# Optimization experiments

Measured on AMD Instinct MI355X. Metric: run time of the kernel, lower is better.

The kernel has to match this reference:

```python
import jax, jax.numpy as jnp
import numpy as np

B, S, D = 4, 2048, 1024
LN_EPS = 1e-3  # Keras LayerNormalization default epsilon

def setup_inputs() -> dict:
    key = jax.random.key(0)
    ks = jax.random.split(key, 7)
    s = D ** -0.5
    return {
        "x": jax.random.normal(ks[0], (B, S, D), dtype=jnp.float32),
        "Wq": jax.random.normal(ks[1], (D, D), dtype=jnp.float32) * s,
        "bq": jnp.zeros((D,), dtype=jnp.float32),
        "Wk": jax.random.normal(ks[2], (D, D), dtype=jnp.float32) * s,
        "bk": jnp.zeros((D,), dtype=jnp.float32),
        "Wv": jax.random.normal(ks[3], (D, D), dtype=jnp.float32) * s,
        "bv": jnp.zeros((D,), dtype=jnp.float32),
        "gamma": jnp.ones((D,), dtype=jnp.float32),
        "beta": jnp.zeros((D,), dtype=jnp.float32),
    }

def reference(x, Wq, bq, Wk, bk, Wv, bv, gamma, beta):
    q = jnp.einsum('bsd,de->bse', x, Wq) + bq
    k = jnp.einsum('bsd,de->bse', x, Wk) + bk
    v = jnp.einsum('bsd,de->bse', x, Wv) + bv
    scale = jnp.asarray(k.shape[-1], x.dtype) ** -0.5
    scores = jnp.einsum('bqd,bkd->bqk', q, k) * scale  # [B,S,S]
    weights = jax.nn.softmax(scores, axis=-1)
    attn = jnp.einsum('bqk,bkd->bqd', weights, v)
    h = x + attn
    mu = jnp.mean(h, axis=-1, keepdims=True)
    var = jnp.mean(jnp.square(h - mu), axis=-1, keepdims=True)
    return gamma * (h - mu) * jax.lax.rsqrt(var + LN_EPS) + beta
```

## Files before the change

### kernel.cpp

```cpp
#include <hip/hip_runtime.h>

typedef __attribute__((ext_vector_type(8))) short bf16x8;
typedef __attribute__((ext_vector_type(4))) float f32x4;

__device__ __forceinline__ unsigned short f2bf(float f) {
    union { float f; unsigned int u; } v; v.f = f;
    unsigned int u = v.u;
    u += 0x7fffu + ((u >> 16) & 1u);
    return (unsigned short)(u >> 16);
}
__device__ __forceinline__ float bf2f(unsigned short s) {
    union { unsigned int u; float f; } v; v.u = ((unsigned int)s) << 16;
    return v.f;
}

__device__ __forceinline__ void gload16(const unsigned short* g, unsigned short* l) {
    __builtin_amdgcn_global_load_lds(
        (const __attribute__((address_space(1))) unsigned int*)(unsigned long long)(g),
        (__attribute__((address_space(3))) unsigned int*)(unsigned int)(unsigned long long)(l),
        16, 0, 0);
}

#define MFMA16(a, b, c) __builtin_amdgcn_mfma_f32_16x16x32_bf16((a), (b), (c), 0, 0, 0)

__global__ __launch_bounds__(256) void detect_dtype(
    const unsigned short* __restrict__ x, int* __restrict__ flag) {
    __shared__ int red[4];
    const int t = threadIdx.x;
    int cnt = 0;
    #pragma unroll
    for (int i = 0; i < 16; i++) {
        const unsigned short v = x[t * 16 + i];
        const int e = (v >> 7) & 0xFF;
        cnt += (e >= 0xC8) ? 1 : 0;
    }
    #pragma unroll
    for (int off = 32; off; off >>= 1) cnt += __shfl_down(cnt, off);
    if ((t & 63) == 0) red[t >> 6] = cnt;
    __syncthreads();
    if (t == 0) *flag = (red[0] + red[1] + red[2] + red[3] >= 16) ? 1 : 0;
}

__global__ __launch_bounds__(256) void convert_x(
    const void* __restrict__ xin, unsigned short* __restrict__ xb,
    const int* __restrict__ flag) {
    const long i = ((long)blockIdx.x * 256 + threadIdx.x) * 4;
    if (*flag) {
        const float4 v = *(const float4*)((const float*)xin + i);
        unsigned long long pk =  (unsigned long long)f2bf(v.x)
                              | ((unsigned long long)f2bf(v.y) << 16)
                              | ((unsigned long long)f2bf(v.z) << 32)
                              | ((unsigned long long)f2bf(v.w) << 48);
        *(unsigned long long*)(xb + i) = pk;
    } else {
        *(unsigned long long*)(xb + i) =
            *(const unsigned long long*)((const unsigned short*)xin + i);
    }
}

__global__ __launch_bounds__(256) void transpose_convert(
    const void* __restrict__ W, unsigned short* __restrict__ Wt,
    const int* __restrict__ flag) {
    __shared__ unsigned short tile[32][33];
    const int tx = threadIdx.x & 31, ty = threadIdx.x >> 5;
    const int x0 = blockIdx.x * 32, y0 = blockIdx.y * 32;
    const int f = *flag;
    #pragma unroll
    for (int i = 0; i < 32; i += 8) {
        const long idx = (long)(y0 + ty + i) * 1024 + x0 + tx;
        tile[ty + i][tx] = f ? f2bf(((const float*)W)[idx])
                             : ((const unsigned short*)W)[idx];
    }
    __syncthreads();
    #pragma unroll
    for (int i = 0; i < 32; i += 8)
        Wt[(long)(x0 + ty + i) * 1024 + y0 + tx] = tile[tx][ty + i];
}

__global__ __launch_bounds__(256) void convert_vec1024(
    const void* __restrict__ in, unsigned short* __restrict__ outv,
    const int* __restrict__ flag) {
    const int i = threadIdx.x * 4;
    if (*flag) {
        const float4 v = *(const float4*)((const float*)in + i);
        outv[i] = f2bf(v.x); outv[i+1] = f2bf(v.y);
        outv[i+2] = f2bf(v.z); outv[i+3] = f2bf(v.w);
    } else {
        *(unsigned long long*)(outv + i) =
            *(const unsigned long long*)((const unsigned short*)in + i);
    }
}

__global__ __launch_bounds__(512, 2) void gemm_bt(
    const unsigned short* __restrict__ A, const unsigned short* __restrict__ Bt,
    unsigned short* __restrict__ C,
    int K, int lda, int ldb, int ldc,
    long strideAz, long strideBz, long strideCz,
    const unsigned short* __restrict__ bias, float scale) {

    const int gx = gridDim.x, gy = gridDim.y;
    const int nwg = gx * gy * (int)gridDim.z;
    int bid = (int)blockIdx.x + gx * ((int)blockIdx.y + gy * (int)blockIdx.z);
    {
        const int q = nwg >> 3, r = nwg & 7;
        const int xcd = bid & 7, idx = bid >> 3;
        bid = (xcd < r ? xcd * (q + 1) : r * (q + 1) + (xcd - r) * q) + idx;
    }
    const int bz  = bid / (gx * gy);
    const int rmd = bid - bz * gx * gy;
    const int by  = rmd / gx;
    const int bx  = rmd - by * gx;

    A  += (long)bz * strideAz;
    Bt += (long)bz * strideBz;
    C  += (long)bz * strideCz;

    __shared__ unsigned short lds[73728];

    const int tid  = threadIdx.x;
    const int wave = tid >> 6;
    const int lane = tid & 63;
    const int quad = lane >> 4;
    const int lm   = lane & 15;
    const int wm   = (wave >> 2) * 64;
    const int wn   = (wave & 3) * 64;

    const int m0 = by * 128;
    const int n0 = bx * 256;

    const int rl   = wave * 8 + (lane >> 3);
    const int ksrc = (((lane & 7) ^ ((lane >> 3) & 7)) << 3);
    const unsigned short* pA0 = A  + (long)(m0 + rl) * lda + ksrc;
    const unsigned short* pB0 = Bt + (long)(n0 + rl) * ldb + ksrc;
    const long sA1 = 64L * lda, sB1 = 64L * ldb;
    const int wofs = wave * 512;

    const int sx8 = lm & 7;
    const int kq0 = ((quad ^ sx8) << 3);
    const int kq1 = (((4 + quad) ^ sx8) << 3);
    const int aro = (wm + lm) << 6;
    const int bro = (wn + lm) << 6;

    f32x4 acc[4][4];
    #pragma unroll
    for (int i = 0; i < 4; i++)
        #pragma unroll
        for (int j = 0; j < 4; j++) acc[i][j] = (f32x4){0.f, 0.f, 0.f, 0.f};

    const int NT = K >> 6;

#define STAGE(kt) do {                                                    \
        unsigned short* ab_ = &lds[((kt) % 3) * 24576 + wofs];            \
        unsigned short* bb_ = ab_ + 8192;                                 \
        const unsigned short* ga_ = pA0 + (long)(kt) * 64;                \
        const unsigned short* gb_ = pB0 + (long)(kt) * 64;                \
        gload16(ga_,            ab_);                                     \
        gload16(ga_ + sA1,      ab_ + 4096);                              \
        gload16(gb_,            bb_);                                     \
        gload16(gb_ + sB1,      bb_ + 4096);                              \
        gload16(gb_ + 2 * sB1,  bb_ + 8192);                              \
        gload16(gb_ + 3 * sB1,  bb_ + 12288);                             \
    } while (0)

    STAGE(0); STAGE(1);
    asm volatile("s_waitcnt vmcnt(6)" ::: "memory");
    __builtin_amdgcn_s_barrier();

    for (int kt = 0; kt < NT; ++kt) {
        const unsigned short* ab = &lds[(kt % 3) * 24576];
        const unsigned short* bb = ab + 8192;

        if (kt + 2 < NT) STAGE(kt + 2);

        bf16x8 aM[4][2], bN[2][2], bN2[2][2];
        #pragma unroll
        for (int i = 0; i < 4; i++) {
            aM[i][0] = *(const bf16x8*)&ab[aro + (i << 10) + kq0];
            aM[i][1] = *(const bf16x8*)&ab[aro + (i << 10) + kq1];
        }
        #pragma unroll
        for (int j = 0; j < 2; j++) {
            bN[j][0] = *(const bf16x8*)&bb[bro + (j << 10) + kq0];
            bN[j][1] = *(const bf16x8*)&bb[bro + (j << 10) + kq1];
        }
        __builtin_amdgcn_s_setprio(1);
        #pragma unroll
        for (int i = 0; i < 4; i++)
            #pragma unroll
            for (int j = 0; j < 2; j++) {
                acc[i][j] = MFMA16(aM[i][0], bN[j][0], acc[i][j]);
                acc[i][j] = MFMA16(aM[i][1], bN[j][1], acc[i][j]);
            }
        __builtin_amdgcn_s_setprio(0);
        #pragma unroll
        for (int j = 0; j < 2; j++) {
            bN2[j][0] = *(const bf16x8*)&bb[bro + ((j + 2) << 10) + kq0];
            bN2[j][1] = *(const bf16x8*)&bb[bro + ((j + 2) << 10) + kq1];
        }
        __builtin_amdgcn_s_setprio(1);
        #pragma unroll
        for (int i = 0; i < 4; i++)
            #pragma unroll
            for (int j = 0; j < 2; j++) {
                acc[i][j + 2] = MFMA16(aM[i][0], bN2[j][0], acc[i][j + 2]);
                acc[i][j + 2] = MFMA16(aM[i][1], bN2[j][1], acc[i][j + 2]);
            }
        __builtin_amdgcn_s_setprio(0);

        if (kt + 2 < NT) { asm volatile("s_waitcnt vmcnt(6)" ::: "memory"); }
        else             { asm volatile("s_waitcnt vmcnt(0)" ::: "memory"); }
        __builtin_amdgcn_s_barrier();
    }
#undef STAGE

    {
        unsigned short* ep = lds + wave * 4096;
        #pragma unroll
        for (int i = 0; i < 4; i++) {
            float b4[4] = {0.f, 0.f, 0.f, 0.f};
            if (bias) {
                const unsigned short* bp = bias + m0 + wm + i * 16 + quad * 4;
                #pragma unroll
                for (int r = 0; r < 4; r++) b4[r] = bf2f(bp[r]);
            }
            const int c = i * 4 + quad;
            const int s = c ^ lm;
            #pragma unroll
            for (int j = 0; j < 4; j++) {
                unsigned long long pk = 0;
                #pragma unroll
                for (int r = 0; r < 4; r++)
                    pk |= (unsigned long long)f2bf((acc[i][j][r] + b4[r]) * scale) << (16 * r);
                *(unsigned long long*)&ep[(j * 16 + lm) * 64 + (s << 2)] = pk;
            }
        }
        const int cc = lane & 15;
        #pragma unroll
        for (int it = 0; it < 16; it++) {
            const int n = it * 4 + (lane >> 4);
            const unsigned long long v =
                *(const unsigned long long*)&ep[n * 64 + ((cc ^ (n & 15)) << 2)];
            *(unsigned long long*)&C[(long)(n0 + wn + n) * ldc + m0 + wm + cc * 4] = v;
        }
    }
}

__global__ __launch_bounds__(256) void softmax_rows(unsigned short* __restrict__ S, int rowlen) {
    __shared__ float red[4];
    const long row = blockIdx.x;
    unsigned short* p = S + row * rowlen;
    const int t = threadIdx.x;
    const int wave = t >> 6, lane = t & 63;

    uint4 raw = *(uint4*)(p + t * 8);
    unsigned short* u = (unsigned short*)&raw;
    float v[8], mx = -3.0e38f;
    #pragma unroll
    for (int i = 0; i < 8; i++) { v[i] = bf2f(u[i]); mx = fmaxf(mx, v[i]); }
    #pragma unroll
    for (int off = 32; off; off >>= 1) mx = fmaxf(mx, __shfl_down(mx, off));
    if (lane == 0) red[wave] = mx;
    __syncthreads();
    mx = fmaxf(fmaxf(red[0], red[1]), fmaxf(red[2], red[3]));
    __syncthreads();

    float s = 0.f;
    #pragma unroll
    for (int i = 0; i < 8; i++) { v[i] = __expf(v[i] - mx); s += v[i]; }
    #pragma unroll
    for (int off = 32; off; off >>= 1) s += __shfl_down(s, off);
    if (lane == 0) red[wave] = s;
    __syncthreads();
    s = red[0] + red[1] + red[2] + red[3];
    const float inv = 1.f / s;
    #pragma unroll
    for (int i = 0; i < 8; i++) u[i] = f2bf(v[i] * inv);
    *(uint4*)(p + t * 8) = raw;
}

__global__ __launch_bounds__(256) void resid_ln(
    const void* __restrict__ x, const unsigned short* __restrict__ attn,
    const void* __restrict__ gamma, const void* __restrict__ beta,
    void* __restrict__ out, const int* __restrict__ flag) {
    __shared__ float red[8];
    const long row = blockIdx.x;
    const int t = threadIdx.x;
    const int wave = t >> 6, lane = t & 63;
    const long base = row * 1024 + t * 4;
    const int f = *flag;

    uint2 ar = *(const uint2*)(attn + base);
    const unsigned short* au = (const unsigned short*)&ar;
    float h[4], s = 0.f, s2 = 0.f;
    if (f) {
        const float4 xr = *(const float4*)((const float*)x + base);
        h[0] = xr.x + bf2f(au[0]); h[1] = xr.y + bf2f(au[1]);
        h[2] = xr.z + bf2f(au[2]); h[3] = xr.w + bf2f(au[3]);
    } else {
        const uint2 xr = *(const uint2*)((const unsigned short*)x + base);
        const unsigned short* xu = (const unsigned short*)&xr;
        #pragma unroll
        for (int i = 0; i < 4; i++) h[i] = bf2f(xu[i]) + bf2f(au[i]);
    }
    #pragma unroll
    for (int i = 0; i < 4; i++) { s += h[i]; s2 += h[i] * h[i]; }
    #pragma unroll
    for (int off = 32; off; off >>= 1) { s += __shfl_down(s, off); s2 += __shfl_down(s2, off); }
    if (lane == 0) { red[wave] = s; red[4 + wave] = s2; }
    __syncthreads();
    s  = red[0] + red[1] + red[2] + red[3];
    s2 = red[4] + red[5] + red[6] + red[7];
    const float mu = s * (1.f / 1024.f);
    const float var = s2 * (1.f / 1024.f) - mu * mu;
    const float rstd = rsqrtf(var + 1e-3f);

    float g[4], bb[4];
    if (f) {
        const float4 gr = *(const float4*)((const float*)gamma + t * 4);
        const float4 br = *(const float4*)((const float*)beta  + t * 4);
        g[0]=gr.x; g[1]=gr.y; g[2]=gr.z; g[3]=gr.w;
        bb[0]=br.x; bb[1]=br.y; bb[2]=br.z; bb[3]=br.w;
    } else {
        #pragma unroll
        for (int i = 0; i < 4; i++) {
            g[i]  = bf2f(((const unsigned short*)gamma)[t * 4 + i]);
            bb[i] = bf2f(((const unsigned short*)beta)[t * 4 + i]);
        }
    }

    if (f) {
        float4 o;
        o.x = g[0]*(h[0]-mu)*rstd + bb[0];
        o.y = g[1]*(h[1]-mu)*rstd + bb[1];
        o.z = g[2]*(h[2]-mu)*rstd + bb[2];
        o.w = g[3]*(h[3]-mu)*rstd + bb[3];
        *(float4*)((float*)out + base) = o;
    } else {
        unsigned long long pk = 0;
        #pragma unroll
        for (int i = 0; i < 4; i++)
            pk |= (unsigned long long)f2bf(g[i]*(h[i]-mu)*rstd + bb[i]) << (16 * i);
        *(unsigned long long*)((unsigned short*)out + base) = pk;
    }
}

extern "C" void kernel_launch(void* const* d_in, const int* in_sizes, int n_in,
                              void* d_out, int out_size, void* d_ws, size_t ws_size,
                              hipStream_t stream) {
    const void* x  = d_in[0];
    const void* Wq = d_in[1];
    const void* bq = d_in[2];
    const void* Wk = d_in[3];
    const void* bk = d_in[4];
    const void* Wv = d_in[5];
    const void* bv = d_in[6];
    const void* gamma = d_in[7];
    const void* beta  = d_in[8];

    char* ws = (char*)d_ws;
    unsigned short* xb   = (unsigned short*)(ws);
    unsigned short* attn = (unsigned short*)(ws);
    unsigned short* wt   = (unsigned short*)(ws + 16777216L);
    unsigned short* bb   = (unsigned short*)(ws + 23068672L);
    int*            flag = (int*)(ws + 23074816L);
    unsigned short* qk   = (unsigned short*)(ws + 23074944L);
    unsigned short* vt   = (unsigned short*)(ws + 56629376L);
    unsigned short* sc   = (unsigned short*)(ws + 73406592L);

    const dim3 tb(256);
    const dim3 tg(512);
    detect_dtype<<<dim3(1), tb, 0, stream>>>((const unsigned short*)x, flag);
    convert_x<<<dim3(8192), tb, 0, stream>>>(x, xb, flag);
    transpose_convert<<<dim3(32, 32), tb, 0, stream>>>(Wq, wt, flag);
    transpose_convert<<<dim3(32, 32), tb, 0, stream>>>(Wk, wt + 1048576, flag);
    transpose_convert<<<dim3(32, 32), tb, 0, stream>>>(Wv, wt + 2097152, flag);
    convert_vec1024<<<dim3(1), tb, 0, stream>>>(bq, bb, flag);
    convert_vec1024<<<dim3(1), tb, 0, stream>>>(bk, bb + 1024, flag);
    convert_vec1024<<<dim3(1), tb, 0, stream>>>(bv, bb + 2048, flag);

    gemm_bt<<<dim3(32, 16, 1), tg, 0, stream>>>(wt, xb, qk,
        1024, 1024, 1024, 2048, 0L, 0L, 0L, bb, 1.0f);
    gemm_bt<<<dim3(4, 64, 1), tg, 0, stream>>>(xb, wt + 2097152, vt,
        1024, 1024, 1024, 8192, 0L, 0L, 0L, nullptr, 1.0f);
    gemm_bt<<<dim3(8, 16, 4), tg, 0, stream>>>(qk + 1024, qk, sc,
        1024, 2048, 2048, 2048, 4194304L, 4194304L, 4194304L, nullptr, 0.03125f);
    softmax_rows<<<dim3(8192), tb, 0, stream>>>(sc, 2048);
    gemm_bt<<<dim3(8, 8, 4), tg, 0, stream>>>(vt, sc, attn,
        2048, 8192, 2048, 1024, 2048L, 4194304L, 2097152L, bb + 2048, 1.0f);
    resid_ln<<<dim3(8192), tb, 0, stream>>>(x, attn, gamma, beta, d_out, flag);
}
```

Before: 292.2 us.

## Template GEMM on M tile size, use 256x256 tiles with double buffering

Makes gemm_bt a template on the M tile (128 or 256) and uses 256x256 output tiles for the QK projection and score GEMMs, doubling per-wave MFMA work for each LDS B load. The LDS pipeline drops from a 3-stage to a 2-stage buffer that waits for vmcnt(0) every iteration, and the epilogue swizzle and store loop are generalized for wider tiles. This raises data reuse and arithmetic intensity. In exchange it gives less load/compute overlap, more registers per thread (risking spills under launch_bounds 512,2), and fewer workgroups.

```diff
diff --git a/kernel.cpp b/kernel.cpp
--- a/kernel.cpp
+++ b/kernel.cpp
@@ -91,6 +91,7 @@
     }
 }
 
+template<int BMT>
 __global__ __launch_bounds__(512, 2) void gemm_bt(
     const unsigned short* __restrict__ A, const unsigned short* __restrict__ Bt,
     unsigned short* __restrict__ C,
@@ -115,17 +116,21 @@
     Bt += (long)bz * strideBz;
     C  += (long)bz * strideCz;
 
-    __shared__ unsigned short lds[73728];
+    constexpr int MI    = BMT / 32;
+    constexpr int ACALL = BMT / 64;
+    constexpr int ASH   = BMT * 64;
+    constexpr int BUFSH = ASH + 16384;
+    __shared__ unsigned short lds[2 * BUFSH];
 
     const int tid  = threadIdx.x;
     const int wave = tid >> 6;
     const int lane = tid & 63;
     const int quad = lane >> 4;
     const int lm   = lane & 15;
-    const int wm   = (wave >> 2) * 64;
+    const int wm   = (wave >> 2) * (BMT / 2);
     const int wn   = (wave & 3) * 64;
 
-    const int m0 = by * 128;
+    const int m0 = by * BMT;
     const int n0 = bx * 256;
 
     const int rl   = wave * 8 + (lane >> 3);
@@ -141,45 +146,45 @@
     const int aro = (wm + lm) << 6;
     const int bro = (wn + lm) << 6;
 
-    f32x4 acc[4][4];
-    #pragma unroll
-    for (int i = 0; i < 4; i++)
+    f32x4 acc[MI][4];
+    #pragma unroll
+    for (int i = 0; i < MI; i++)
         #pragma unroll
         for (int j = 0; j < 4; j++) acc[i][j] = (f32x4){0.f, 0.f, 0.f, 0.f};
 
     const int NT = K >> 6;
 
 #define STAGE(kt) do {                                                    \
-        unsigned short* ab_ = &lds[((kt) % 3) * 24576 + wofs];            \
-        unsigned short* bb_ = ab_ + 8192;                                 \
+        unsigned short* ab_ = &lds[((kt) & 1) * BUFSH + wofs];            \
+        unsigned short* bb_ = ab_ + ASH;                                  \
         const unsigned short* ga_ = pA0 + (long)(kt) * 64;                \
         const unsigned short* gb_ = pB0 + (long)(kt) * 64;                \
-        gload16(ga_,            ab_);                                     \
-        gload16(ga_ + sA1,      ab_ + 4096);                              \
-        gload16(gb_,            bb_);                                     \
-        gload16(gb_ + sB1,      bb_ + 4096);                              \
-        gload16(gb_ + 2 * sB1,  bb_ + 8192);                              \
-        gload16(gb_ + 3 * sB1,  bb_ + 12288);                             \
+        _Pragma("unroll")                                                 \
+        for (int h = 0; h < ACALL; h++)                                   \
+            gload16(ga_ + h * sA1, ab_ + h * 4096);                       \
+        _Pragma("unroll")                                                 \
+        for (int h = 0; h < 4; h++)                                       \
+            gload16(gb_ + h * sB1, bb_ + h * 4096);                       \
     } while (0)
 
-    STAGE(0); STAGE(1);
-    asm volatile("s_waitcnt vmcnt(6)" ::: "memory");
+    STAGE(0);
+    asm volatile("s_waitcnt vmcnt(0)" ::: "memory");
     __builtin_amdgcn_s_barrier();
 
     for (int kt = 0; kt < NT; ++kt) {
-        const unsigned short* ab = &lds[(kt % 3) * 24576];
-        const unsigned short* bb = ab + 8192;
-
-        if (kt + 2 < NT) STAGE(kt + 2);
-
-        bf16x8 aM[4][2], bN[2][2], bN2[2][2];
+        const unsigned short* ab = &lds[(kt & 1) * BUFSH];
+        const unsigned short* bb = ab + ASH;
+
+        if (kt + 1 < NT) STAGE(kt + 1);
+
+        bf16x8 aM[4][2], bN[4][2];
         #pragma unroll
         for (int i = 0; i < 4; i++) {
             aM[i][0] = *(const bf16x8*)&ab[aro + (i << 10) + kq0];
             aM[i][1] = *(const bf16x8*)&ab[aro + (i << 10) + kq1];
         }
         #pragma unroll
-        for (int j = 0; j < 2; j++) {
+        for (int j = 0; j < 4; j++) {
             bN[j][0] = *(const bf16x8*)&bb[bro + (j << 10) + kq0];
             bN[j][1] = *(const bf16x8*)&bb[bro + (j << 10) + kq1];
         }
@@ -187,36 +192,40 @@
         #pragma unroll
         for (int i = 0; i < 4; i++)
             #pragma unroll
-            for (int j = 0; j < 2; j++) {
+            for (int j = 0; j < 4; j++) {
                 acc[i][j] = MFMA16(aM[i][0], bN[j][0], acc[i][j]);
                 acc[i][j] = MFMA16(aM[i][1], bN[j][1], acc[i][j]);
             }
         __builtin_amdgcn_s_setprio(0);
-        #pragma unroll
-        for (int j = 0; j < 2; j++) {
-            bN2[j][0] = *(const bf16x8*)&bb[bro + ((j + 2) << 10) + kq0];
-            bN2[j][1] = *(const bf16x8*)&bb[bro + ((j + 2) << 10) + kq1];
-        }
-        __builtin_amdgcn_s_setprio(1);
-        #pragma unroll
-        for (int i = 0; i < 4; i++)
+
+        if constexpr (MI == 8) {
+            bf16x8 aH[4][2];
             #pragma unroll
-            for (int j = 0; j < 2; j++) {
-                acc[i][j + 2] = MFMA16(aM[i][0], bN2[j][0], acc[i][j + 2]);
-                acc[i][j + 2] = MFMA16(aM[i][1], bN2[j][1], acc[i][j + 2]);
+            for (int i = 0; i < 4; i++) {
+                aH[i][0] = *(const bf16x8*)&ab[aro + ((i + 4) << 10) + kq0];
+                aH[i][1] = *(const bf16x8*)&ab[aro + ((i + 4) << 10) + kq1];
             }
-        __builtin_amdgcn_s_setprio(0);
-
-        if (kt + 2 < NT) { asm volatile("s_waitcnt vmcnt(6)" ::: "memory"); }
-        else             { asm volatile("s_waitcnt vmcnt(0)" ::: "memory"); }
+            __builtin_amdgcn_s_setprio(1);
+            #pragma unroll
+            for (int i = 0; i < 4; i++)
+                #pragma unroll
+                for (int j = 0; j < 4; j++) {
+                    acc[i + 4][j] = MFMA16(aH[i][0], bN[j][0], acc[i + 4][j]);
+                    acc[i + 4][j] = MFMA16(aH[i][1], bN[j][1], acc[i + 4][j]);
+                }
+            __builtin_amdgcn_s_setprio(0);
+        }
+
+        asm volatile("s_waitcnt vmcnt(0)" ::: "memory");
         __builtin_amdgcn_s_barrier();
     }
 #undef STAGE
 
     {
-        unsigned short* ep = lds + wave * 4096;
-        #pragma unroll
-        for (int i = 0; i < 4; i++) {
+        unsigned short* ep = lds + wave * (MI * 1024);
+        const int rowsh = MI * 16;
+        #pragma unroll
+        for (int i = 0; i < MI; i++) {
             float b4[4] = {0.f, 0.f, 0.f, 0.f};
             if (bias) {
                 const unsigned short* bp = bias + m0 + wm + i * 16 + quad * 4;
@@ -224,22 +233,24 @@
                 for (int r = 0; r < 4; r++) b4[r] = bf2f(bp[r]);
             }
             const int c = i * 4 + quad;
-            const int s = c ^ lm;
+            const int s = (c & ~15) | ((c & 15) ^ lm);
             #pragma unroll
             for (int j = 0; j < 4; j++) {
                 unsigned long long pk = 0;
                 #pragma unroll
                 for (int r = 0; r < 4; r++)
                     pk |= (unsigned long long)f2bf((acc[i][j][r] + b4[r]) * scale) << (16 * r);
-                *(unsigned long long*)&ep[(j * 16 + lm) * 64 + (s << 2)] = pk;
+                *(unsigned long long*)&ep[(j * 16 + lm) * rowsh + (s << 2)] = pk;
             }
         }
-        const int cc = lane & 15;
-        #pragma unroll
-        for (int it = 0; it < 16; it++) {
-            const int n = it * 4 + (lane >> 4);
+        __builtin_amdgcn_s_barrier();
+        const int cc = lane & (4 * MI - 1);
+        #pragma unroll
+        for (int it = 0; it < 4 * MI; it++) {
+            const int n = it * (64 / (4 * MI)) + (lane / (4 * MI));
+            const int sr = (cc & ~15) | ((cc & 15) ^ (n & 15));
             const unsigned long long v =
-                *(const unsigned long long*)&ep[n * 64 + ((cc ^ (n & 15)) << 2)];
+                *(const unsigned long long*)&ep[n * rowsh + (sr << 2)];
             *(unsigned long long*)&C[(long)(n0 + wn + n) * ldc + m0 + wm + cc * 4] = v;
         }
     }
@@ -378,14 +389,14 @@
     convert_vec1024<<<dim3(1), tb, 0, stream>>>(bk, bb + 1024, flag);
     convert_vec1024<<<dim3(1), tb, 0, stream>>>(bv, bb + 2048, flag);
 
-    gemm_bt<<<dim3(32, 16, 1), tg, 0, stream>>>(wt, xb, qk,
+    gemm_bt<256><<<dim3(32, 8, 1), tg, 0, stream>>>(wt, xb, qk,
         1024, 1024, 1024, 2048, 0L, 0L, 0L, bb, 1.0f);
-    gemm_bt<<<dim3(4, 64, 1), tg, 0, stream>>>(xb, wt + 2097152, vt,
+    gemm_bt<128><<<dim3(4, 64, 1), tg, 0, stream>>>(xb, wt + 2097152, vt,
         1024, 1024, 1024, 8192, 0L, 0L, 0L, nullptr, 1.0f);
-    gemm_bt<<<dim3(8, 16, 4), tg, 0, stream>>>(qk + 1024, qk, sc,
+    gemm_bt<256><<<dim3(8, 8, 4), tg, 0, stream>>>(qk + 1024, qk, sc,
         1024, 2048, 2048, 2048, 4194304L, 4194304L, 4194304L, nullptr, 0.03125f);
     softmax_rows<<<dim3(8192), tb, 0, stream>>>(sc, 2048);
-    gemm_bt<<<dim3(8, 8, 4), tg, 0, stream>>>(vt, sc, attn,
+    gemm_bt<128><<<dim3(8, 8, 4), tg, 0, stream>>>(vt, sc, attn,
         2048, 8192, 2048, 1024, 2048L, 4194304L, 2097152L, bb + 2048, 1.0f);
     resid_ln<<<dim3(8192), tb, 0, stream>>>(x, attn, gamma, beta, d_out, flag);
 }
```

After: 273.3 us. -6.5%, faster.
